# Optimization experiments

Hardware: AMD Instinct MI355X
Metric: run time of the kernel (lower is better)

Reference implementation:

```python
import jax, jax.numpy as jnp
import numpy as np

N_NODES = 50000
N_EDGES = 600000
IN_CH = 64
HID = 128
N_GRAPHS = 64
EPS = 0.0  # GINEConv default eps


def setup_inputs() -> dict:
    key = jax.random.key(0)
    ks = jax.random.split(key, 16)
    x = jax.random.normal(ks[0], (N_NODES, IN_CH), dtype=jnp.float32)
    edge_index = jax.random.randint(ks[1], (2, N_EDGES), 0, N_NODES, dtype=jnp.int64)
    edge_attr = jax.random.normal(ks[2], (N_EDGES, 3), dtype=jnp.float32)
    batch = jnp.sort(jax.random.randint(ks[3], (N_NODES,), 0, N_GRAPHS, dtype=jnp.int64))
    s = lambda fan_in: 1.0 / np.sqrt(fan_in)
    # conv1: edge lin (3->IN_CH), mlp (IN_CH->HID->HID)
    el1_w = jax.random.uniform(ks[4], (3, IN_CH), minval=-s(3), maxval=s(3))
    el1_b = jnp.zeros((IN_CH,), jnp.float32)
    w1a = jax.random.uniform(ks[5], (IN_CH, HID), minval=-s(IN_CH), maxval=s(IN_CH))
    b1a = jnp.zeros((HID,), jnp.float32)
    w1b = jax.random.uniform(ks[6], (HID, HID), minval=-s(HID), maxval=s(HID))
    b1b = jnp.zeros((HID,), jnp.float32)
    # conv2: edge lin (3->HID), mlp (HID->HID->HID)
    el2_w = jax.random.uniform(ks[7], (3, HID), minval=-s(3), maxval=s(3))
    el2_b = jnp.zeros((HID,), jnp.float32)
    w2a = jax.random.uniform(ks[8], (HID, HID), minval=-s(HID), maxval=s(HID))
    b2a = jnp.zeros((HID,), jnp.float32)
    w2b = jax.random.uniform(ks[9], (HID, HID), minval=-s(HID), maxval=s(HID))
    b2b = jnp.zeros((HID,), jnp.float32)
    return dict(x=x, edge_index=edge_index, edge_attr=edge_attr, batch=batch,
                el1_w=el1_w, el1_b=el1_b, w1a=w1a, b1a=b1a, w1b=w1b, b1b=b1b,
                el2_w=el2_w, el2_b=el2_b, w2a=w2a, b2a=b2a, w2b=w2b, b2b=b2b)


def _gine_conv(x, src, dst, edge_attr, el_w, el_b, wa, ba, wb, bb):
    # message: relu(x_j + Lin(edge_attr)), aggregated (sum) at target nodes
    e = edge_attr @ el_w + el_b              # [E, d]
    msg = jax.nn.relu(x[src] + e)            # [E, d]
    agg = jax.ops.segment_sum(msg, dst, num_segments=x.shape[0])  # [N, d]
    h = (1.0 + EPS) * x + agg
    h = jax.nn.relu(h @ wa + ba) @ wb + bb   # MLP
    return h


def reference(x, edge_index, edge_attr, batch,
              el1_w, el1_b, w1a, b1a, w1b, b1b,
              el2_w, el2_b, w2a, b2a, w2b, b2b):
    src, dst = edge_index[0], edge_index[1]
    h = jax.nn.relu(_gine_conv(x, src, dst, edge_attr, el1_w, el1_b, w1a, b1a, w1b, b1b))
    h = jax.nn.relu(_gine_conv(h, src, dst, edge_attr, el2_w, el2_b, w2a, b2a, w2b, b2b))
    # global mean pool per graph
    sums = jax.ops.segment_sum(h, batch, num_segments=N_GRAPHS)
    cnt = jax.ops.segment_sum(jnp.ones((h.shape[0],), h.dtype), batch, num_segments=N_GRAPHS)
    return sums / jnp.maximum(cnt, 1.0)[:, None]
```

## Files before the change

kernel.cpp:

```cpp
#include <hip/hip_runtime.h>

#define N_NODES 50000
#define N_EDGES 600000
#define N_PAD 50048
#define IN_CH 64
#define HID 128
#define N_GRAPHS 64
#define CAP 64
#define CAP_SHIFT 6

typedef __attribute__((ext_vector_type(8))) short bf16x8;
typedef __attribute__((ext_vector_type(4))) float f32x4;

__device__ __forceinline__ float bf2f(unsigned short u) {
    union { unsigned int i; float f; } v; v.i = ((unsigned int)u) << 16; return v.f;
}
__device__ __forceinline__ unsigned short f2bf(float f) {
    union { float f; unsigned int i; } v; v.f = f;
    unsigned int u = v.i;
    return (unsigned short)((u + 0x7FFFu + ((u >> 16) & 1u)) >> 16);
}


__global__ void prep_kernel(const float* __restrict__ x,
                            const float* __restrict__ w1a, const float* __restrict__ w1b,
                            const float* __restrict__ w2a, const float* __restrict__ w2b,
                            unsigned short* __restrict__ xbf,
                            unsigned short* __restrict__ waT1, unsigned short* __restrict__ wbT1,
                            unsigned short* __restrict__ waT2, unsigned short* __restrict__ wbT2,
                            int* __restrict__ deg, float* __restrict__ psum) {
    int i = blockIdx.x * blockDim.x + threadIdx.x;
    if (i < N_NODES * IN_CH) xbf[i] = f2bf(x[i]);
    if (i < N_NODES) deg[i] = 0;
    if (i < N_GRAPHS * HID) psum[i] = 0.f;
    if (i < IN_CH * HID) {
        int k = i / HID, n = i % HID;
        waT1[n * IN_CH + k] = f2bf(w1a[i]);
    }
    if (i < HID * HID) {
        int k = i / HID, n = i % HID;
        wbT1[n * HID + k] = f2bf(w1b[i]);
        waT2[n * HID + k] = f2bf(w2a[i]);
        wbT2[n * HID + k] = f2bf(w2b[i]);
    }
}

__global__ void build_kernel(const int* __restrict__ ei,
                             const float* __restrict__ ea,
                             int* __restrict__ deg,
                             uint2* __restrict__ edata) {
    int i = blockIdx.x * blockDim.x + threadIdx.x;
    if (i >= N_EDGES) return;
    int s = ei[i];
    int d = ei[N_EDGES + i];
    float a0 = ea[3 * (size_t)i], a1 = ea[3 * (size_t)i + 1], a2 = ea[3 * (size_t)i + 2];
    int p = atomicAdd(&deg[d], 1);
    if (p < CAP)
        edata[((size_t)d << CAP_SHIFT) + p] =
            make_uint2((unsigned)s | ((unsigned)f2bf(a0) << 16),
                       (unsigned)f2bf(a1) | ((unsigned)f2bf(a2) << 16));
}

__global__ void gather64_kernel(const unsigned short* __restrict__ xin,
                                const uint2* __restrict__ edata,
                                const int* __restrict__ deg,
                                const float* __restrict__ elw,
                                const float* __restrict__ elb,
                                unsigned short* __restrict__ sg) {
    constexpr int K = IN_CH;
    constexpr int NPB = 4;
    const int node0 = blockIdx.x * NPB;
    const int t = threadIdx.x;
    const int c = t & 63, half = t >> 6;
    const float w0 = elw[c], w1 = elw[K + c], w2 = elw[2 * K + c], eb = elb[c];

    auto term = [&](uint2 e, unsigned short row) -> float {
        float ev = bf2f((unsigned short)(e.x >> 16)) * w0 +
                   bf2f((unsigned short)(e.y & 0xFFFF)) * w1 +
                   bf2f((unsigned short)(e.y >> 16)) * w2 + eb;
        float m = bf2f(row) + ev;
        return m > 0.f ? m : 0.f;
    };

    for (int i = 0; i < NPB; i += 2) {
        int node = node0 + i + half;
        float acc = bf2f(xin[(size_t)node * K + c]);
        int dn = deg[node]; if (dn > CAP) dn = CAP;
        int jb = node << CAP_SHIFT, je = jb + dn;
        int j = jb;
        for (; j + 8 <= je; j += 8) {
            uint2 e0 = edata[j],     e1 = edata[j + 1], e2 = edata[j + 2], e3 = edata[j + 3];
            uint2 e4 = edata[j + 4], e5 = edata[j + 5], e6 = edata[j + 6], e7 = edata[j + 7];
            unsigned short r0 = xin[(size_t)(e0.x & 0xFFFF) * K + c];
            unsigned short r1 = xin[(size_t)(e1.x & 0xFFFF) * K + c];
            unsigned short r2 = xin[(size_t)(e2.x & 0xFFFF) * K + c];
            unsigned short r3 = xin[(size_t)(e3.x & 0xFFFF) * K + c];
            unsigned short r4 = xin[(size_t)(e4.x & 0xFFFF) * K + c];
            unsigned short r5 = xin[(size_t)(e5.x & 0xFFFF) * K + c];
            unsigned short r6 = xin[(size_t)(e6.x & 0xFFFF) * K + c];
            unsigned short r7 = xin[(size_t)(e7.x & 0xFFFF) * K + c];
            acc += term(e0, r0) + term(e1, r1) + term(e2, r2) + term(e3, r3)
                 + term(e4, r4) + term(e5, r5) + term(e6, r6) + term(e7, r7);
        }
        for (; j + 4 <= je; j += 4) {
            uint2 e0 = edata[j], e1 = edata[j + 1], e2 = edata[j + 2], e3 = edata[j + 3];
            unsigned short r0 = xin[(size_t)(e0.x & 0xFFFF) * K + c];
            unsigned short r1 = xin[(size_t)(e1.x & 0xFFFF) * K + c];
            unsigned short r2 = xin[(size_t)(e2.x & 0xFFFF) * K + c];
            unsigned short r3 = xin[(size_t)(e3.x & 0xFFFF) * K + c];
            acc += term(e0, r0) + term(e1, r1) + term(e2, r2) + term(e3, r3);
        }
        for (; j < je; j++) {
            uint2 e0 = edata[j];
            acc += term(e0, xin[(size_t)(e0.x & 0xFFFF) * K + c]);
        }
        sg[(size_t)node * K + c] = f2bf(acc);
    }
}

__global__ void gather128_kernel(const unsigned short* __restrict__ xin,
                                 const uint2* __restrict__ edata,
                                 const int* __restrict__ deg,
                                 const float* __restrict__ elw,
                                 const float* __restrict__ elb,
                                 unsigned short* __restrict__ sg) {
    const int t = threadIdx.x;
    const int w = t >> 6, l = t & 63;
    const unsigned* x32 = (const unsigned*)xin;
    unsigned* sg32 = (unsigned*)sg;
    const int c0 = 2 * l;
    const float w00 = elw[c0],           w01 = elw[c0 + 1];
    const float w10 = elw[HID + c0],     w11 = elw[HID + c0 + 1];
    const float w20 = elw[2 * HID + c0], w21 = elw[2 * HID + c0 + 1];
    const float eb0 = elb[c0],           eb1 = elb[c0 + 1];
    const int nA = (blockIdx.x * 4 + w) * 2;
    const int nB = nA + 1;

    unsigned svA = x32[(size_t)nA * 64 + l];
    unsigned svB = x32[(size_t)nB * 64 + l];
    float a0 = bf2f((unsigned short)(svA & 0xFFFF));
    float a1 = bf2f((unsigned short)(svA >> 16));
    float b0 = bf2f((unsigned short)(svB & 0xFFFF));
    float b1 = bf2f((unsigned short)(svB >> 16));

    auto term2 = [&](uint2 e, unsigned r, float& p0, float& p1) {
        float A0 = bf2f((unsigned short)(e.x >> 16));
        float A1 = bf2f((unsigned short)(e.y & 0xFFFF));
        float A2 = bf2f((unsigned short)(e.y >> 16));
        float ev0 = A0 * w00 + A1 * w10 + A2 * w20 + eb0;
        float ev1 = A0 * w01 + A1 * w11 + A2 * w21 + eb1;
        float m0 = bf2f((unsigned short)(r & 0xFFFF)) + ev0;
        float m1 = bf2f((unsigned short)(r >> 16)) + ev1;
        p0 += m0 > 0.f ? m0 : 0.f;
        p1 += m1 > 0.f ? m1 : 0.f;
    };

    int dA = deg[nA]; if (dA > CAP) dA = CAP;
    int dB = deg[nB]; if (dB > CAP) dB = CAP;
    int ja = nA << CAP_SHIFT; const int jaE = ja + dA;
    int jb = nB << CAP_SHIFT; const int jbE = jb + dB;
    while (ja + 4 <= jaE && jb + 4 <= jbE) {
        uint2 eA0 = edata[ja],     eA1 = edata[ja + 1], eA2 = edata[ja + 2], eA3 = edata[ja + 3];
        uint2 eB0 = edata[jb],     eB1 = edata[jb + 1], eB2 = edata[jb + 2], eB3 = edata[jb + 3];
        unsigned rA0 = x32[(size_t)(eA0.x & 0xFFFF) * 64 + l];
        unsigned rA1 = x32[(size_t)(eA1.x & 0xFFFF) * 64 + l];
        unsigned rA2 = x32[(size_t)(eA2.x & 0xFFFF) * 64 + l];
        unsigned rA3 = x32[(size_t)(eA3.x & 0xFFFF) * 64 + l];
        unsigned rB0 = x32[(size_t)(eB0.x & 0xFFFF) * 64 + l];
        unsigned rB1 = x32[(size_t)(eB1.x & 0xFFFF) * 64 + l];
        unsigned rB2 = x32[(size_t)(eB2.x & 0xFFFF) * 64 + l];
        unsigned rB3 = x32[(size_t)(eB3.x & 0xFFFF) * 64 + l];
        term2(eA0, rA0, a0, a1); term2(eA1, rA1, a0, a1);
        term2(eA2, rA2, a0, a1); term2(eA3, rA3, a0, a1);
        term2(eB0, rB0, b0, b1); term2(eB1, rB1, b0, b1);
        term2(eB2, rB2, b0, b1); term2(eB3, rB3, b0, b1);
        ja += 4; jb += 4;
    }
    for (; ja + 4 <= jaE; ja += 4) {
        uint2 e0 = edata[ja], e1 = edata[ja + 1], e2 = edata[ja + 2], e3 = edata[ja + 3];
        unsigned r0 = x32[(size_t)(e0.x & 0xFFFF) * 64 + l];
        unsigned r1 = x32[(size_t)(e1.x & 0xFFFF) * 64 + l];
        unsigned r2 = x32[(size_t)(e2.x & 0xFFFF) * 64 + l];
        unsigned r3 = x32[(size_t)(e3.x & 0xFFFF) * 64 + l];
        term2(e0, r0, a0, a1); term2(e1, r1, a0, a1);
        term2(e2, r2, a0, a1); term2(e3, r3, a0, a1);
    }
    for (; ja < jaE; ja++) {
        uint2 e0 = edata[ja];
        term2(e0, x32[(size_t)(e0.x & 0xFFFF) * 64 + l], a0, a1);
    }
    for (; jb + 4 <= jbE; jb += 4) {
        uint2 e0 = edata[jb], e1 = edata[jb + 1], e2 = edata[jb + 2], e3 = edata[jb + 3];
        unsigned r0 = x32[(size_t)(e0.x & 0xFFFF) * 64 + l];
        unsigned r1 = x32[(size_t)(e1.x & 0xFFFF) * 64 + l];
        unsigned r2 = x32[(size_t)(e2.x & 0xFFFF) * 64 + l];
        unsigned r3 = x32[(size_t)(e3.x & 0xFFFF) * 64 + l];
        term2(e0, r0, b0, b1); term2(e1, r1, b0, b1);
        term2(e2, r2, b0, b1); term2(e3, r3, b0, b1);
    }
    for (; jb < jbE; jb++) {
        uint2 e0 = edata[jb];
        term2(e0, x32[(size_t)(e0.x & 0xFFFF) * 64 + l], b0, b1);
    }
    sg32[(size_t)nA * 64 + l] = (unsigned)f2bf(a0) | ((unsigned)f2bf(a1) << 16);
    sg32[(size_t)nB * 64 + l] = (unsigned)f2bf(b0) | ((unsigned)f2bf(b1) << 16);
}

template <int K, bool POOL>
__global__ __launch_bounds__(256)
void mlp_mfma_kernel(const unsigned short* __restrict__ sg,
                     const unsigned short* __restrict__ waT,
                     const float* __restrict__ ba,
                     const unsigned short* __restrict__ wbT,
                     const float* __restrict__ bb,
                     void* __restrict__ outv,
                     const int* __restrict__ batch) {
    constexpr int HSTR = 136;
    constexpr int OSTR = HID + 4;
    __shared__ __align__(16) unsigned short sHid[4][16 * HSTR];
    __shared__ __align__(16) float sOut[64 * OSTR];
    const int t = threadIdx.x;
    const int w = t >> 6, l = t & 63;
    const int i16 = l & 15, q = l >> 4;
    const int blk0 = blockIdx.x * 64;
    const int row0 = blk0 + w * 16;

    bf16x8 aA[K / 32];
    #pragma unroll
    for (int s = 0; s < K / 32; s++)
        aA[s] = *(const bf16x8*)&sg[(size_t)(row0 + i16) * K + s * 32 + q * 8];
    unsigned short* myHid = sHid[w];
    #pragma unroll
    for (int ct = 0; ct < 8; ct++) {
        int col = ct * 16 + i16;
        float bv = ba[col];
        f32x4 acc = (f32x4){bv, bv, bv, bv};
        #pragma unroll
        for (int s = 0; s < K / 32; s++) {
            bf16x8 b = *(const bf16x8*)&waT[(size_t)col * K + s * 32 + q * 8];
            acc = __builtin_amdgcn_mfma_f32_16x16x32_bf16(aA[s], b, acc, 0, 0, 0);
        }
        #pragma unroll
        for (int r = 0; r < 4; r++) {
            float v = acc[r] > 0.f ? acc[r] : 0.f;
            myHid[(q * 4 + r) * HSTR + col] = f2bf(v);
        }
    }
    __syncthreads();

    bf16x8 aB[4];
    #pragma unroll
    for (int s = 0; s < 4; s++)
        aB[s] = *(const bf16x8*)&myHid[i16 * HSTR + s * 32 + q * 8];
    #pragma unroll
    for (int ct = 0; ct < 8; ct++) {
        int col = ct * 16 + i16;
        float bv = bb[col];
        f32x4 acc = (f32x4){bv, bv, bv, bv};
        #pragma unroll
        for (int s = 0; s < 4; s++) {
            bf16x8 b = *(const bf16x8*)&wbT[(size_t)col * HID + s * 32 + q * 8];
            acc = __builtin_amdgcn_mfma_f32_16x16x32_bf16(aB[s], b, acc, 0, 0, 0);
        }
        #pragma unroll
        for (int r = 0; r < 4; r++) {
            float v = acc[r] > 0.f ? acc[r] : 0.f;
            sOut[(w * 16 + q * 4 + r) * OSTR + col] = v;
        }
    }
    __syncthreads();

    if (POOL) {
        if (t < HID) {
            float* psum = (float*)outv;
            float acc = 0.f;
            int curg = batch[blk0];
            for (int row = 0; row < 64; row++) {
                int node = blk0 + row;
                if (node >= N_NODES) break;
                int g = batch[node];
                if (g != curg) {
                    atomicAdd(&psum[curg * HID + t], acc);
                    acc = 0.f; curg = g;
                }
                acc += sOut[row * OSTR + t];
            }
            atomicAdd(&psum[curg * HID + t], acc);
        }
    } else {
        unsigned short* hout = (unsigned short*)outv;
        for (int idx = t; idx < 64 * 16; idx += 256) {
            int row = idx >> 4, ch = idx & 15;
            int node = blk0 + row;
            if (node < N_NODES) {
                float4 f0 = *(const float4*)&sOut[row * OSTR + ch * 8];
                float4 f1 = *(const float4*)&sOut[row * OSTR + ch * 8 + 4];
                uint4 u;
                u.x = (unsigned)f2bf(f0.x) | ((unsigned)f2bf(f0.y) << 16);
                u.y = (unsigned)f2bf(f0.z) | ((unsigned)f2bf(f0.w) << 16);
                u.z = (unsigned)f2bf(f1.x) | ((unsigned)f2bf(f1.y) << 16);
                u.w = (unsigned)f2bf(f1.z) | ((unsigned)f2bf(f1.w) << 16);
                *(uint4*)&hout[(size_t)node * HID + ch * 8] = u;
            }
        }
    }
}

__global__ void pool_div_kernel(const float* __restrict__ sums,
                                const int* __restrict__ batch,
                                float* __restrict__ out) {
    int i = blockIdx.x * blockDim.x + threadIdx.x;
    if (i >= N_GRAPHS * HID) return;
    int g = i / HID;
    int lo = 0, hi = N_NODES;
    while (lo < hi) { int mid = (lo + hi) >> 1; if (batch[mid] < g) lo = mid + 1; else hi = mid; }
    int start = lo;
    lo = 0; hi = N_NODES;
    while (lo < hi) { int mid = (lo + hi) >> 1; if (batch[mid] <= g) lo = mid + 1; else hi = mid; }
    float c = (float)(lo - start);
    out[i] = sums[i] / (c > 1.0f ? c : 1.0f);
}

extern "C" void kernel_launch(void* const* d_in, const int* in_sizes, int n_in,
                              void* d_out, int out_size, void* d_ws, size_t ws_size,
                              hipStream_t stream) {
    const float* x    = (const float*)d_in[0];
    const int*   ei   = (const int*)d_in[1];
    const float* ea   = (const float*)d_in[2];
    const int*   batch= (const int*)d_in[3];
    const float* el1w = (const float*)d_in[4];
    const float* el1b = (const float*)d_in[5];
    const float* w1a  = (const float*)d_in[6];
    const float* b1a  = (const float*)d_in[7];
    const float* w1b  = (const float*)d_in[8];
    const float* b1b  = (const float*)d_in[9];
    const float* el2w = (const float*)d_in[10];
    const float* el2b = (const float*)d_in[11];
    const float* w2a  = (const float*)d_in[12];
    const float* b2a  = (const float*)d_in[13];
    const float* w2b  = (const float*)d_in[14];
    const float* b2b  = (const float*)d_in[15];
    float* out = (float*)d_out;

    uint2* edata    = (uint2*)d_ws;
    float* psum     = (float*)(edata + (size_t)N_NODES * CAP);
    int*   deg      = (int*)(psum + N_GRAPHS * HID);
    unsigned short* hbf  = (unsigned short*)((char*)psum + (size_t)58192 * 4);
    unsigned short* sgbuf= hbf + (size_t)N_NODES * HID;
    unsigned short* waT1 = sgbuf + (size_t)N_PAD * HID;
    unsigned short* wbT1 = waT1 + HID * IN_CH;
    unsigned short* waT2 = wbT1 + HID * HID;
    unsigned short* wbT2 = waT2 + HID * HID;
    unsigned short* xbf  = wbT2 + HID * HID;

    prep_kernel<<<(N_NODES * IN_CH) / 256, 256, 0, stream>>>(
        x, w1a, w1b, w2a, w2b, xbf, waT1, wbT1, waT2, wbT2, deg, psum);
    build_kernel<<<(N_EDGES + 255) / 256, 256, 0, stream>>>(ei, ea, deg, edata);

    gather64_kernel<<<N_NODES / 4, 128, 0, stream>>>(
        xbf, edata, deg, el1w, el1b, sgbuf);
    mlp_mfma_kernel<IN_CH, false><<<N_PAD / 64, 256, 0, stream>>>(
        sgbuf, waT1, b1a, wbT1, b1b, hbf, nullptr);

    gather128_kernel<<<N_NODES / 8, 256, 0, stream>>>(
        hbf, edata, deg, el2w, el2b, sgbuf);
    mlp_mfma_kernel<HID, true><<<N_PAD / 64, 256, 0, stream>>>(
        sgbuf, waT2, b2a, wbT2, b2b, psum, batch);

    pool_div_kernel<<<(N_GRAPHS * HID + 255) / 256, 256, 0, stream>>>(psum, batch, out);
}
```

Before: 268.7 us.

## Fuse neighbor gather with MFMA MLP into one kernel per GINE layer

```diff
diff --git a/kernel.cpp b/kernel.cpp
--- a/kernel.cpp
+++ b/kernel.cpp
@@ -61,175 +61,170 @@
                        (unsigned)f2bf(a1) | ((unsigned)f2bf(a2) << 16));
 }
 
-__global__ void gather64_kernel(const unsigned short* __restrict__ xin,
-                                const uint2* __restrict__ edata,
-                                const int* __restrict__ deg,
-                                const float* __restrict__ elw,
-                                const float* __restrict__ elb,
-                                unsigned short* __restrict__ sg) {
-    constexpr int K = IN_CH;
-    constexpr int NPB = 4;
-    const int node0 = blockIdx.x * NPB;
-    const int t = threadIdx.x;
-    const int c = t & 63, half = t >> 6;
-    const float w0 = elw[c], w1 = elw[K + c], w2 = elw[2 * K + c], eb = elb[c];
-
-    auto term = [&](uint2 e, unsigned short row) -> float {
-        float ev = bf2f((unsigned short)(e.x >> 16)) * w0 +
-                   bf2f((unsigned short)(e.y & 0xFFFF)) * w1 +
-                   bf2f((unsigned short)(e.y >> 16)) * w2 + eb;
-        float m = bf2f(row) + ev;
-        return m > 0.f ? m : 0.f;
-    };
-
-    for (int i = 0; i < NPB; i += 2) {
-        int node = node0 + i + half;
-        float acc = bf2f(xin[(size_t)node * K + c]);
-        int dn = deg[node]; if (dn > CAP) dn = CAP;
-        int jb = node << CAP_SHIFT, je = jb + dn;
-        int j = jb;
-        for (; j + 8 <= je; j += 8) {
-            uint2 e0 = edata[j],     e1 = edata[j + 1], e2 = edata[j + 2], e3 = edata[j + 3];
-            uint2 e4 = edata[j + 4], e5 = edata[j + 5], e6 = edata[j + 6], e7 = edata[j + 7];
-            unsigned short r0 = xin[(size_t)(e0.x & 0xFFFF) * K + c];
-            unsigned short r1 = xin[(size_t)(e1.x & 0xFFFF) * K + c];
-            unsigned short r2 = xin[(size_t)(e2.x & 0xFFFF) * K + c];
-            unsigned short r3 = xin[(size_t)(e3.x & 0xFFFF) * K + c];
-            unsigned short r4 = xin[(size_t)(e4.x & 0xFFFF) * K + c];
-            unsigned short r5 = xin[(size_t)(e5.x & 0xFFFF) * K + c];
-            unsigned short r6 = xin[(size_t)(e6.x & 0xFFFF) * K + c];
-            unsigned short r7 = xin[(size_t)(e7.x & 0xFFFF) * K + c];
-            acc += term(e0, r0) + term(e1, r1) + term(e2, r2) + term(e3, r3)
-                 + term(e4, r4) + term(e5, r5) + term(e6, r6) + term(e7, r7);
-        }
-        for (; j + 4 <= je; j += 4) {
-            uint2 e0 = edata[j], e1 = edata[j + 1], e2 = edata[j + 2], e3 = edata[j + 3];
-            unsigned short r0 = xin[(size_t)(e0.x & 0xFFFF) * K + c];
-            unsigned short r1 = xin[(size_t)(e1.x & 0xFFFF) * K + c];
-            unsigned short r2 = xin[(size_t)(e2.x & 0xFFFF) * K + c];
-            unsigned short r3 = xin[(size_t)(e3.x & 0xFFFF) * K + c];
-            acc += term(e0, r0) + term(e1, r1) + term(e2, r2) + term(e3, r3);
-        }
-        for (; j < je; j++) {
-            uint2 e0 = edata[j];
-            acc += term(e0, xin[(size_t)(e0.x & 0xFFFF) * K + c]);
-        }
-        sg[(size_t)node * K + c] = f2bf(acc);
-    }
-}
-
-__global__ void gather128_kernel(const unsigned short* __restrict__ xin,
-                                 const uint2* __restrict__ edata,
-                                 const int* __restrict__ deg,
-                                 const float* __restrict__ elw,
-                                 const float* __restrict__ elb,
-                                 unsigned short* __restrict__ sg) {
-    const int t = threadIdx.x;
-    const int w = t >> 6, l = t & 63;
-    const unsigned* x32 = (const unsigned*)xin;
-    unsigned* sg32 = (unsigned*)sg;
-    const int c0 = 2 * l;
-    const float w00 = elw[c0],           w01 = elw[c0 + 1];
-    const float w10 = elw[HID + c0],     w11 = elw[HID + c0 + 1];
-    const float w20 = elw[2 * HID + c0], w21 = elw[2 * HID + c0 + 1];
-    const float eb0 = elb[c0],           eb1 = elb[c0 + 1];
-    const int nA = (blockIdx.x * 4 + w) * 2;
-    const int nB = nA + 1;
-
-    unsigned svA = x32[(size_t)nA * 64 + l];
-    unsigned svB = x32[(size_t)nB * 64 + l];
-    float a0 = bf2f((unsigned short)(svA & 0xFFFF));
-    float a1 = bf2f((unsigned short)(svA >> 16));
-    float b0 = bf2f((unsigned short)(svB & 0xFFFF));
-    float b1 = bf2f((unsigned short)(svB >> 16));
-
-    auto term2 = [&](uint2 e, unsigned r, float& p0, float& p1) {
-        float A0 = bf2f((unsigned short)(e.x >> 16));
-        float A1 = bf2f((unsigned short)(e.y & 0xFFFF));
-        float A2 = bf2f((unsigned short)(e.y >> 16));
-        float ev0 = A0 * w00 + A1 * w10 + A2 * w20 + eb0;
-        float ev1 = A0 * w01 + A1 * w11 + A2 * w21 + eb1;
-        float m0 = bf2f((unsigned short)(r & 0xFFFF)) + ev0;
-        float m1 = bf2f((unsigned short)(r >> 16)) + ev1;
-        p0 += m0 > 0.f ? m0 : 0.f;
-        p1 += m1 > 0.f ? m1 : 0.f;
-    };
-
-    int dA = deg[nA]; if (dA > CAP) dA = CAP;
-    int dB = deg[nB]; if (dB > CAP) dB = CAP;
-    int ja = nA << CAP_SHIFT; const int jaE = ja + dA;
-    int jb = nB << CAP_SHIFT; const int jbE = jb + dB;
-    while (ja + 4 <= jaE && jb + 4 <= jbE) {
-        uint2 eA0 = edata[ja],     eA1 = edata[ja + 1], eA2 = edata[ja + 2], eA3 = edata[ja + 3];
-        uint2 eB0 = edata[jb],     eB1 = edata[jb + 1], eB2 = edata[jb + 2], eB3 = edata[jb + 3];
-        unsigned rA0 = x32[(size_t)(eA0.x & 0xFFFF) * 64 + l];
-        unsigned rA1 = x32[(size_t)(eA1.x & 0xFFFF) * 64 + l];
-        unsigned rA2 = x32[(size_t)(eA2.x & 0xFFFF) * 64 + l];
-        unsigned rA3 = x32[(size_t)(eA3.x & 0xFFFF) * 64 + l];
-        unsigned rB0 = x32[(size_t)(eB0.x & 0xFFFF) * 64 + l];
-        unsigned rB1 = x32[(size_t)(eB1.x & 0xFFFF) * 64 + l];
-        unsigned rB2 = x32[(size_t)(eB2.x & 0xFFFF) * 64 + l];
-        unsigned rB3 = x32[(size_t)(eB3.x & 0xFFFF) * 64 + l];
-        term2(eA0, rA0, a0, a1); term2(eA1, rA1, a0, a1);
-        term2(eA2, rA2, a0, a1); term2(eA3, rA3, a0, a1);
-        term2(eB0, rB0, b0, b1); term2(eB1, rB1, b0, b1);
-        term2(eB2, rB2, b0, b1); term2(eB3, rB3, b0, b1);
-        ja += 4; jb += 4;
-    }
-    for (; ja + 4 <= jaE; ja += 4) {
-        uint2 e0 = edata[ja], e1 = edata[ja + 1], e2 = edata[ja + 2], e3 = edata[ja + 3];
-        unsigned r0 = x32[(size_t)(e0.x & 0xFFFF) * 64 + l];
-        unsigned r1 = x32[(size_t)(e1.x & 0xFFFF) * 64 + l];
-        unsigned r2 = x32[(size_t)(e2.x & 0xFFFF) * 64 + l];
-        unsigned r3 = x32[(size_t)(e3.x & 0xFFFF) * 64 + l];
-        term2(e0, r0, a0, a1); term2(e1, r1, a0, a1);
-        term2(e2, r2, a0, a1); term2(e3, r3, a0, a1);
-    }
-    for (; ja < jaE; ja++) {
-        uint2 e0 = edata[ja];
-        term2(e0, x32[(size_t)(e0.x & 0xFFFF) * 64 + l], a0, a1);
-    }
-    for (; jb + 4 <= jbE; jb += 4) {
-        uint2 e0 = edata[jb], e1 = edata[jb + 1], e2 = edata[jb + 2], e3 = edata[jb + 3];
-        unsigned r0 = x32[(size_t)(e0.x & 0xFFFF) * 64 + l];
-        unsigned r1 = x32[(size_t)(e1.x & 0xFFFF) * 64 + l];
-        unsigned r2 = x32[(size_t)(e2.x & 0xFFFF) * 64 + l];
-        unsigned r3 = x32[(size_t)(e3.x & 0xFFFF) * 64 + l];
-        term2(e0, r0, b0, b1); term2(e1, r1, b0, b1);
-        term2(e2, r2, b0, b1); term2(e3, r3, b0, b1);
-    }
-    for (; jb < jbE; jb++) {
-        uint2 e0 = edata[jb];
-        term2(e0, x32[(size_t)(e0.x & 0xFFFF) * 64 + l], b0, b1);
-    }
-    sg32[(size_t)nA * 64 + l] = (unsigned)f2bf(a0) | ((unsigned)f2bf(a1) << 16);
-    sg32[(size_t)nB * 64 + l] = (unsigned)f2bf(b0) | ((unsigned)f2bf(b1) << 16);
-}
-
 template <int K, bool POOL>
 __global__ __launch_bounds__(256)
-void mlp_mfma_kernel(const unsigned short* __restrict__ sg,
-                     const unsigned short* __restrict__ waT,
-                     const float* __restrict__ ba,
-                     const unsigned short* __restrict__ wbT,
-                     const float* __restrict__ bb,
-                     void* __restrict__ outv,
-                     const int* __restrict__ batch) {
+void gine_fused_kernel(const unsigned short* __restrict__ xin,
+                       const uint2* __restrict__ edata,
+                       const int* __restrict__ deg,
+                       const float* __restrict__ elw,
+                       const float* __restrict__ elb,
+                       const unsigned short* __restrict__ waT,
+                       const float* __restrict__ ba,
+                       const unsigned short* __restrict__ wbT,
+                       const float* __restrict__ bb,
+                       void* __restrict__ outv,
+                       const int* __restrict__ batch) {
+    constexpr int SSTR = K + 8;
     constexpr int HSTR = 136;
     constexpr int OSTR = HID + 4;
-    __shared__ __align__(16) unsigned short sHid[4][16 * HSTR];
-    __shared__ __align__(16) float sOut[64 * OSTR];
+    constexpr int SG_B  = 64 * SSTR * 2;
+    constexpr int HID_B = 4 * 16 * HSTR * 2;
+    constexpr int OUT_B = 64 * OSTR * 4;
+    constexpr int TOT_B = (SG_B + HID_B > OUT_B) ? (SG_B + HID_B) : OUT_B;
+    __shared__ __align__(16) char lds[TOT_B];
+    unsigned short* sgT  = (unsigned short*)lds;
+    unsigned short* sHid = (unsigned short*)(lds + SG_B);
+    float* sOut = (float*)lds;
+
     const int t = threadIdx.x;
     const int w = t >> 6, l = t & 63;
     const int i16 = l & 15, q = l >> 4;
     const int blk0 = blockIdx.x * 64;
-    const int row0 = blk0 + w * 16;
+    const int lrow0 = w * 16;
+    const int node0 = blk0 + lrow0;
+
+    if constexpr (K == IN_CH) {
+        const float w0 = elw[l], w1 = elw[K + l], w2 = elw[2 * K + l], eb = elb[l];
+        auto term = [&](uint2 e, unsigned short row) -> float {
+            float ev = bf2f((unsigned short)(e.x >> 16)) * w0 +
+                       bf2f((unsigned short)(e.y & 0xFFFF)) * w1 +
+                       bf2f((unsigned short)(e.y >> 16)) * w2 + eb;
+            float m = bf2f(row) + ev;
+            return m > 0.f ? m : 0.f;
+        };
+        for (int i = 0; i < 16; i++) {
+            int node = node0 + i;
+            if (node >= N_NODES) break;
+            float acc = bf2f(xin[(size_t)node * K + l]);
+            int dn = deg[node]; if (dn > CAP) dn = CAP;
+            int j = node << CAP_SHIFT; const int je = j + dn;
+            for (; j + 8 <= je; j += 8) {
+                uint2 e0 = edata[j],     e1 = edata[j + 1], e2 = edata[j + 2], e3 = edata[j + 3];
+                uint2 e4 = edata[j + 4], e5 = edata[j + 5], e6 = edata[j + 6], e7 = edata[j + 7];
+                unsigned short r0 = xin[(size_t)(e0.x & 0xFFFF) * K + l];
+                unsigned short r1 = xin[(size_t)(e1.x & 0xFFFF) * K + l];
+                unsigned short r2 = xin[(size_t)(e2.x & 0xFFFF) * K + l];
+                unsigned short r3 = xin[(size_t)(e3.x & 0xFFFF) * K + l];
+                unsigned short r4 = xin[(size_t)(e4.x & 0xFFFF) * K + l];
+                unsigned short r5 = xin[(size_t)(e5.x & 0xFFFF) * K + l];
+                unsigned short r6 = xin[(size_t)(e6.x & 0xFFFF) * K + l];
+                unsigned short r7 = xin[(size_t)(e7.x & 0xFFFF) * K + l];
+                acc += term(e0, r0) + term(e1, r1) + term(e2, r2) + term(e3, r3)
+                     + term(e4, r4) + term(e5, r5) + term(e6, r6) + term(e7, r7);
+            }
+            for (; j + 4 <= je; j += 4) {
+                uint2 e0 = edata[j], e1 = edata[j + 1], e2 = edata[j + 2], e3 = edata[j + 3];
+                unsigned short r0 = xin[(size_t)(e0.x & 0xFFFF) * K + l];
+                unsigned short r1 = xin[(size_t)(e1.x & 0xFFFF) * K + l];
+                unsigned short r2 = xin[(size_t)(e2.x & 0xFFFF) * K + l];
+                unsigned short r3 = xin[(size_t)(e3.x & 0xFFFF) * K + l];
+                acc += term(e0, r0) + term(e1, r1) + term(e2, r2) + term(e3, r3);
+            }
+            for (; j < je; j++) {
+                uint2 e0 = edata[j];
+                acc += term(e0, xin[(size_t)(e0.x & 0xFFFF) * K + l]);
+            }
+            sgT[(lrow0 + i) * SSTR + l] = f2bf(acc);
+        }
+    } else {
+        const unsigned* x32 = (const unsigned*)xin;
+        unsigned* sgT32 = (unsigned*)sgT;
+        constexpr int S32 = SSTR / 2;
+        const int c0 = 2 * l;
+        const float w00 = elw[c0],           w01 = elw[c0 + 1];
+        const float w10 = elw[HID + c0],     w11 = elw[HID + c0 + 1];
+        const float w20 = elw[2 * HID + c0], w21 = elw[2 * HID + c0 + 1];
+        const float eb0 = elb[c0],           eb1 = elb[c0 + 1];
+
+        auto term2 = [&](uint2 e, unsigned r, float& p0, float& p1) {
+            float A0 = bf2f((unsigned short)(e.x >> 16));
+            float A1 = bf2f((unsigned short)(e.y & 0xFFFF));
+            float A2 = bf2f((unsigned short)(e.y >> 16));
+            float ev0 = A0 * w00 + A1 * w10 + A2 * w20 + eb0;
+            float ev1 = A0 * w01 + A1 * w11 + A2 * w21 + eb1;
+            float m0 = bf2f((unsigned short)(r & 0xFFFF)) + ev0;
+            float m1 = bf2f((unsigned short)(r >> 16)) + ev1;
+            p0 += m0 > 0.f ? m0 : 0.f;
+            p1 += m1 > 0.f ? m1 : 0.f;
+        };
+
+        for (int p = 0; p < 8; p++) {
+            int nA = node0 + 2 * p, nB = nA + 1;
+            if (nA >= N_NODES) break;
+            unsigned svA = x32[(size_t)nA * 64 + l];
+            unsigned svB = x32[(size_t)nB * 64 + l];
+            float a0 = bf2f((unsigned short)(svA & 0xFFFF));
+            float a1 = bf2f((unsigned short)(svA >> 16));
+            float b0 = bf2f((unsigned short)(svB & 0xFFFF));
+            float b1 = bf2f((unsigned short)(svB >> 16));
+
+            int dA = deg[nA]; if (dA > CAP) dA = CAP;
+            int dB = deg[nB]; if (dB > CAP) dB = CAP;
+            int ja = nA << CAP_SHIFT; const int jaE = ja + dA;
+            int jb = nB << CAP_SHIFT; const int jbE = jb + dB;
+            while (ja + 4 <= jaE && jb + 4 <= jbE) {
+                uint2 eA0 = edata[ja],     eA1 = edata[ja + 1], eA2 = edata[ja + 2], eA3 = edata[ja + 3];
+                uint2 eB0 = edata[jb],     eB1 = edata[jb + 1], eB2 = edata[jb + 2], eB3 = edata[jb + 3];
+                unsigned rA0 = x32[(size_t)(eA0.x & 0xFFFF) * 64 + l];
+                unsigned rA1 = x32[(size_t)(eA1.x & 0xFFFF) * 64 + l];
+                unsigned rA2 = x32[(size_t)(eA2.x & 0xFFFF) * 64 + l];
+                unsigned rA3 = x32[(size_t)(eA3.x & 0xFFFF) * 64 + l];
+                unsigned rB0 = x32[(size_t)(eB0.x & 0xFFFF) * 64 + l];
+                unsigned rB1 = x32[(size_t)(eB1.x & 0xFFFF) * 64 + l];
+                unsigned rB2 = x32[(size_t)(eB2.x & 0xFFFF) * 64 + l];
+                unsigned rB3 = x32[(size_t)(eB3.x & 0xFFFF) * 64 + l];
+                term2(eA0, rA0, a0, a1); term2(eA1, rA1, a0, a1);
+                term2(eA2, rA2, a0, a1); term2(eA3, rA3, a0, a1);
+                term2(eB0, rB0, b0, b1); term2(eB1, rB1, b0, b1);
+                term2(eB2, rB2, b0, b1); term2(eB3, rB3, b0, b1);
+                ja += 4; jb += 4;
+            }
+            for (; ja + 4 <= jaE; ja += 4) {
+                uint2 e0 = edata[ja], e1 = edata[ja + 1], e2 = edata[ja + 2], e3 = edata[ja + 3];
+                unsigned r0 = x32[(size_t)(e0.x & 0xFFFF) * 64 + l];
+                unsigned r1 = x32[(size_t)(e1.x & 0xFFFF) * 64 + l];
+                unsigned r2 = x32[(size_t)(e2.x & 0xFFFF) * 64 + l];
+                unsigned r3 = x32[(size_t)(e3.x & 0xFFFF) * 64 + l];
+                term2(e0, r0, a0, a1); term2(e1, r1, a0, a1);
+                term2(e2, r2, a0, a1); term2(e3, r3, a0, a1);
+            }
+            for (; ja < jaE; ja++) {
+                uint2 e0 = edata[ja];
+                term2(e0, x32[(size_t)(e0.x & 0xFFFF) * 64 + l], a0, a1);
+            }
+            for (; jb + 4 <= jbE; jb += 4) {
+                uint2 e0 = edata[jb], e1 = edata[jb + 1], e2 = edata[jb + 2], e3 = edata[jb + 3];
+                unsigned r0 = x32[(size_t)(e0.x & 0xFFFF) * 64 + l];
+                unsigned r1 = x32[(size_t)(e1.x & 0xFFFF) * 64 + l];
+                unsigned r2 = x32[(size_t)(e2.x & 0xFFFF) * 64 + l];
+                unsigned r3 = x32[(size_t)(e3.x & 0xFFFF) * 64 + l];
+                term2(e0, r0, b0, b1); term2(e1, r1, b0, b1);
+                term2(e2, r2, b0, b1); term2(e3, r3, b0, b1);
+            }
+            for (; jb < jbE; jb++) {
+                uint2 e0 = edata[jb];
+                term2(e0, x32[(size_t)(e0.x & 0xFFFF) * 64 + l], b0, b1);
+            }
+            sgT32[(lrow0 + 2 * p) * S32 + l]     = (unsigned)f2bf(a0) | ((unsigned)f2bf(a1) << 16);
+            sgT32[(lrow0 + 2 * p + 1) * S32 + l] = (unsigned)f2bf(b0) | ((unsigned)f2bf(b1) << 16);
+        }
+    }
 
     bf16x8 aA[K / 32];
     #pragma unroll
     for (int s = 0; s < K / 32; s++)
-        aA[s] = *(const bf16x8*)&sg[(size_t)(row0 + i16) * K + s * 32 + q * 8];
-    unsigned short* myHid = sHid[w];
+        aA[s] = *(const bf16x8*)&sgT[(size_t)(lrow0 + i16) * SSTR + s * 32 + q * 8];
+    unsigned short* myHid = sHid + w * (16 * HSTR);
     #pragma unroll
     for (int ct = 0; ct < 8; ct++) {
         int col = ct * 16 + i16;
@@ -246,12 +241,12 @@
             myHid[(q * 4 + r) * HSTR + col] = f2bf(v);
         }
     }
-    __syncthreads();
 
     bf16x8 aB[4];
     #pragma unroll
     for (int s = 0; s < 4; s++)
         aB[s] = *(const bf16x8*)&myHid[i16 * HSTR + s * 32 + q * 8];
+    __syncthreads();
     #pragma unroll
     for (int ct = 0; ct < 8; ct++) {
         int col = ct * 16 + i16;
@@ -265,7 +260,7 @@
         #pragma unroll
         for (int r = 0; r < 4; r++) {
             float v = acc[r] > 0.f ? acc[r] : 0.f;
-            sOut[(w * 16 + q * 4 + r) * OSTR + col] = v;
+            sOut[(lrow0 + q * 4 + r) * OSTR + col] = v;
         }
     }
     __syncthreads();
@@ -346,8 +341,7 @@
     float* psum     = (float*)(edata + (size_t)N_NODES * CAP);
     int*   deg      = (int*)(psum + N_GRAPHS * HID);
     unsigned short* hbf  = (unsigned short*)((char*)psum + (size_t)58192 * 4);
-    unsigned short* sgbuf= hbf + (size_t)N_NODES * HID;
-    unsigned short* waT1 = sgbuf + (size_t)N_PAD * HID;
+    unsigned short* waT1 = hbf + (size_t)N_NODES * HID;
     unsigned short* wbT1 = waT1 + HID * IN_CH;
     unsigned short* waT2 = wbT1 + HID * HID;
     unsigned short* wbT2 = waT2 + HID * HID;
@@ -357,15 +351,11 @@
         x, w1a, w1b, w2a, w2b, xbf, waT1, wbT1, waT2, wbT2, deg, psum);
     build_kernel<<<(N_EDGES + 255) / 256, 256, 0, stream>>>(ei, ea, deg, edata);
 
-    gather64_kernel<<<N_NODES / 4, 128, 0, stream>>>(
-        xbf, edata, deg, el1w, el1b, sgbuf);
-    mlp_mfma_kernel<IN_CH, false><<<N_PAD / 64, 256, 0, stream>>>(
-        sgbuf, waT1, b1a, wbT1, b1b, hbf, nullptr);
-
-    gather128_kernel<<<N_NODES / 8, 256, 0, stream>>>(
-        hbf, edata, deg, el2w, el2b, sgbuf);
-    mlp_mfma_kernel<HID, true><<<N_PAD / 64, 256, 0, stream>>>(
-        sgbuf, waT2, b2a, wbT2, b2b, psum, batch);
+    gine_fused_kernel<IN_CH, false><<<N_PAD / 64, 256, 0, stream>>>(
+        xbf, edata, deg, el1w, el1b, waT1, b1a, wbT1, b1b, hbf, nullptr);
+
+    gine_fused_kernel<HID, true><<<N_PAD / 64, 256, 0, stream>>>(
+        hbf, edata, deg, el2w, el2b, waT2, b2a, wbT2, b2b, psum, batch);
 
     pool_div_kernel<<<(N_GRAPHS * HID + 255) / 256, 256, 0, stream>>>(psum, batch, out);
 }
```

Result: slower. 282.1 us (+5.0%).
